# Kernel tuning notes

Hardware: AMD Instinct MI355X
Metric: run time of the kernel (lower is better)

## Reference

```python
import jax, jax.numpy as jnp
import numpy as np

N = 100000      # nodes per graph batch
E = 1600000     # edges per graph batch
F_IN = 128
HID = 128
N_GRAPHS = 64


def gcn_conv(x, edge_index, W, b):
    """PyG GCNConv: add self-loops, symmetric deg^-1/2 normalization, scatter-add."""
    n = x.shape[0]
    xw = x @ W                                  # [N, H]
    src, dst = edge_index[0], edge_index[1]
    # degree including self-loop
    deg = jnp.zeros((n,), xw.dtype).at[dst].add(jnp.ones((src.shape[0],), xw.dtype)) + 1.0
    dinv = jax.lax.rsqrt(deg)                   # deg^-1/2
    norm = (dinv[src] * dinv[dst])[:, None]     # [E, 1]
    msg = xw[src] * norm                        # gather + scale
    agg = jnp.zeros_like(xw).at[dst].add(msg)   # scatter-add
    agg = agg + xw * (dinv * dinv)[:, None]     # self-loop contribution
    return agg + b


def global_mean_pool(x, batch, num_graphs):
    sums = jax.ops.segment_sum(x, batch, num_segments=num_graphs)
    cnts = jax.ops.segment_sum(jnp.ones((x.shape[0],), x.dtype), batch, num_segments=num_graphs)
    return sums / jnp.maximum(cnts, 1.0)[:, None]


def setup_inputs() -> dict:
    key = jax.random.key(0)
    ks = jax.random.split(key, 16)
    s = 1.0 / np.sqrt(F_IN)
    sh = 1.0 / np.sqrt(HID)
    return {
        "x_H": jax.random.normal(ks[0], (N, F_IN), jnp.float32),
        "edge_index_H": jax.random.randint(ks[1], (2, E), 0, N, jnp.int64),
        "x_G": jax.random.normal(ks[2], (N, F_IN), jnp.float32),
        "edge_index_G": jax.random.randint(ks[3], (2, E), 0, N, jnp.int64),
        "batch_H": jnp.sort(jax.random.randint(ks[4], (N,), 0, N_GRAPHS, jnp.int64)),
        "batch_G": jnp.sort(jax.random.randint(ks[5], (N,), 0, N_GRAPHS, jnp.int64)),
        # selector params
        "sel_W1": jax.random.uniform(ks[6], (F_IN, HID), jnp.float32, -s, s),
        "sel_b1": jnp.zeros((HID,), jnp.float32),
        "sel_W2": jax.random.uniform(ks[7], (HID, HID), jnp.float32, -sh, sh),
        "sel_b2": jnp.zeros((HID,), jnp.float32),
        "sel_fcw": jax.random.uniform(ks[8], (HID, 1), jnp.float32, -sh, sh),
        "sel_fcb": jnp.zeros((1,), jnp.float32),
        # embedder params (shared between F and G branches)
        "emb_W1": jax.random.uniform(ks[9], (F_IN, HID), jnp.float32, -s, s),
        "emb_b1": jnp.zeros((HID,), jnp.float32),
        "emb_W2": jax.random.uniform(ks[10], (HID, HID), jnp.float32, -sh, sh),
        "emb_b2": jnp.zeros((HID,), jnp.float32),
    }


def reference(x_H, edge_index_H, x_G, edge_index_G, batch_H, batch_G,
              sel_W1, sel_b1, sel_W2, sel_b2, sel_fcw, sel_fcb,
              emb_W1, emb_b1, emb_W2, emb_b2):
    # selector on H
    h = jax.nn.relu(gcn_conv(x_H, edge_index_H, sel_W1, sel_b1))
    h = jax.nn.relu(gcn_conv(h, edge_index_H, sel_W2, sel_b2))
    p = jax.nn.sigmoid(h @ sel_fcw + sel_fcb)          # [N, 1]

    def embed(x, ei, batch):
        z = jax.nn.relu(gcn_conv(x, ei, emb_W1, emb_b1))
        z = jax.nn.relu(gcn_conv(z, ei, emb_W2, emb_b2))
        return global_mean_pool(z, batch, N_GRAPHS)

    h_F = embed(x_H * p, edge_index_H, batch_H)
    h_G = embed(x_G, edge_index_G, batch_G)
    return (h_F, h_G, p)
```

## Files before the change

### kernel.cpp

```cpp
#include <hip/hip_runtime.h>
#include <cstdint>
#include <cstddef>

#define FEAT 128
#define PSLICE 8
#define BSHIFT 7
#define CAP 4096

typedef _Float16 h16;
typedef __attribute__((ext_vector_type(8))) _Float16 h16x8;
typedef __attribute__((ext_vector_type(4))) _Float16 h16x4;
typedef __attribute__((ext_vector_type(4))) float f32x4;

__global__ __launch_bounds__(256) void k_cvt(const float* __restrict__ X,
    h16* __restrict__ Y, int nv) {
  int i = blockIdx.x * 256 + threadIdx.x;
  if (i < nv) {
    const float* p = X + (size_t)i * 8;
    float4 a = *(const float4*)p, b = *(const float4*)(p + 4);
    h16x8 o;
    o[0] = (h16)a.x; o[1] = (h16)a.y; o[2] = (h16)a.z; o[3] = (h16)a.w;
    o[4] = (h16)b.x; o[5] = (h16)b.y; o[6] = (h16)b.z; o[7] = (h16)b.w;
    *(h16x8*)&Y[(size_t)i * 8] = o;
  }
}

__global__ __launch_bounds__(256) void k_part(const int* __restrict__ ei,
    unsigned int* __restrict__ pair, int* __restrict__ gcur, int E, int nb) {
  __shared__ int cnt[1024];
  __shared__ int base[1024];
  int per = (E + gridDim.x - 1) / gridDim.x;
  int e0 = blockIdx.x * per;
  int e1 = min(e0 + per, E);
  for (int i = threadIdx.x; i < nb; i += 256) cnt[i] = 0;
  __syncthreads();
  for (int e = e0 + threadIdx.x; e < e1; e += 256)
    atomicAdd(&cnt[ei[E + e] >> BSHIFT], 1);
  __syncthreads();
  for (int i = threadIdx.x; i < nb; i += 256) {
    int c = cnt[i];
    base[i] = c ? atomicAdd(&gcur[i], c) : 0;
    cnt[i] = 0;
  }
  __syncthreads();
  for (int e = e0 + threadIdx.x; e < e1; e += 256) {
    int src = ei[e];
    int dst = ei[E + e];
    int b = dst >> BSHIFT;
    int pos = base[b] + atomicAdd(&cnt[b], 1);
    if (pos < CAP) pair[(size_t)b * CAP + pos] = ((unsigned)src << BSHIFT) | (unsigned)(dst & 127);
  }
}

__global__ __launch_bounds__(1024) void k_bscan(const int* __restrict__ cnt,
    int* __restrict__ boffs, int* __restrict__ offs, int nb, int N, int E) {
  __shared__ int wsum[16];
  __shared__ int carry;
  int tid = threadIdx.x;
  int lane = tid & 63;
  int wid = tid >> 6;
  if (tid == 0) carry = 0;
  for (int base = 0; base < nb; base += 1024) {
    __syncthreads();
    int c0 = carry;
    int i = base + tid;
    int v = (i < nb) ? cnt[i] : 0;
    int x = v;
#pragma unroll
    for (int off = 1; off < 64; off <<= 1) {
      int t = __shfl_up(x, off);
      if (lane >= off) x += t;
    }
    if (lane == 63) wsum[wid] = x;
    __syncthreads();
    if (wid == 0) {
      int t = (lane < 16) ? wsum[lane] : 0;
#pragma unroll
      for (int off = 1; off < 16; off <<= 1) {
        int u = __shfl_up(t, off);
        if (lane >= off) t += u;
      }
      if (lane < 16) wsum[lane] = t;
    }
    __syncthreads();
    int wex = (wid == 0) ? 0 : wsum[wid - 1];
    int o = c0 + wex + (x - v);
    if (i < nb) boffs[i] = o;
    int total = wsum[15];
    __syncthreads();
    if (tid == 0) carry = c0 + total;
  }
  __syncthreads();
  if (tid == 0) { boffs[nb] = carry; offs[N] = E; }
}

__global__ __launch_bounds__(256) void k_bucket(const unsigned int* __restrict__ pair,
    const int* __restrict__ bcnt, const int* __restrict__ boffs,
    int* __restrict__ csr, int* __restrict__ offs, float* __restrict__ dinv,
    int N) {
  int b = blockIdx.x;
  int m = min(bcnt[b], CAP);
  __shared__ int cnt[128];
  __shared__ int noff[128];
  __shared__ int w0tot;
  if (threadIdx.x < 128) cnt[threadIdx.x] = 0;
  __syncthreads();
  const unsigned int* p = pair + (size_t)b * CAP;
  for (int i = threadIdx.x; i < m; i += 256)
    atomicAdd(&cnt[p[i] & 127u], 1);
  __syncthreads();
  int v = 0, x = 0;
  int lane = threadIdx.x & 63, w = threadIdx.x >> 6;
  if (threadIdx.x < 128) {
    v = cnt[threadIdx.x];
    x = v;
#pragma unroll
    for (int o = 1; o < 64; o <<= 1) {
      int t = __shfl_up(x, o);
      if (lane >= o) x += t;
    }
    if (threadIdx.x == 63) w0tot = x;
  }
  __syncthreads();
  int cbase = boffs[b];
  if (threadIdx.x < 128) {
    int ex = x - v + ((w == 1) ? w0tot : 0);
    int g = (b << BSHIFT) + threadIdx.x;
    if (g < N) {
      offs[g] = cbase + ex;
      dinv[g] = 1.0f / sqrtf((float)v + 1.0f);
    }
    noff[threadIdx.x] = ex;
    cnt[threadIdx.x] = 0;
  }
  __syncthreads();
  for (int i = threadIdx.x; i < m; i += 256) {
    unsigned pk = p[i];
    int d = pk & 127u;
    int pos = cbase + noff[d] + atomicAdd(&cnt[d], 1);
    csr[pos] = (int)(pk >> BSHIFT);
  }
}

__global__ __launch_bounds__(256) void k_wprep(const float* __restrict__ W,
    h16* __restrict__ WT) {
  int i = blockIdx.x * 256 + threadIdx.x;
  int k = i >> 7, c = i & 127;
  WT[c * FEAT + k] = (h16)W[(size_t)k * FEAT + c];
}

__device__ inline float4 ldrow4(const h16* p) {
  h16x4 v = *(const h16x4*)p;
  return make_float4((float)v[0], (float)v[1], (float)v[2], (float)v[3]);
}

__device__ inline float4 gather_row(const h16* __restrict__ XW,
    const int* __restrict__ offs, const int* __restrict__ csr, int node, int f) {
  float4 a0 = ldrow4(&XW[(size_t)node * FEAT + f]);
  float4 a1 = {0,0,0,0}, a2 = {0,0,0,0}, a3 = {0,0,0,0};
  float4 a4 = {0,0,0,0}, a5 = {0,0,0,0}, a6 = {0,0,0,0}, a7 = {0,0,0,0};
  int s = offs[node], e = offs[node + 1];
  int i = s;
  for (; i + 8 <= e; i += 8) {
    int s0 = csr[i + 0], s1 = csr[i + 1], s2 = csr[i + 2], s3 = csr[i + 3];
    int s4 = csr[i + 4], s5 = csr[i + 5], s6 = csr[i + 6], s7 = csr[i + 7];
    float4 v0 = ldrow4(&XW[(size_t)s0 * FEAT + f]);
    float4 v1 = ldrow4(&XW[(size_t)s1 * FEAT + f]);
    float4 v2 = ldrow4(&XW[(size_t)s2 * FEAT + f]);
    float4 v3 = ldrow4(&XW[(size_t)s3 * FEAT + f]);
    float4 v4 = ldrow4(&XW[(size_t)s4 * FEAT + f]);
    float4 v5 = ldrow4(&XW[(size_t)s5 * FEAT + f]);
    float4 v6 = ldrow4(&XW[(size_t)s6 * FEAT + f]);
    float4 v7 = ldrow4(&XW[(size_t)s7 * FEAT + f]);
    a0.x += v0.x; a0.y += v0.y; a0.z += v0.z; a0.w += v0.w;
    a1.x += v1.x; a1.y += v1.y; a1.z += v1.z; a1.w += v1.w;
    a2.x += v2.x; a2.y += v2.y; a2.z += v2.z; a2.w += v2.w;
    a3.x += v3.x; a3.y += v3.y; a3.z += v3.z; a3.w += v3.w;
    a4.x += v4.x; a4.y += v4.y; a4.z += v4.z; a4.w += v4.w;
    a5.x += v5.x; a5.y += v5.y; a5.z += v5.z; a5.w += v5.w;
    a6.x += v6.x; a6.y += v6.y; a6.z += v6.z; a6.w += v6.w;
    a7.x += v7.x; a7.y += v7.y; a7.z += v7.z; a7.w += v7.w;
  }
  if (i + 4 <= e) {
    int s0 = csr[i + 0], s1 = csr[i + 1], s2 = csr[i + 2], s3 = csr[i + 3];
    float4 v0 = ldrow4(&XW[(size_t)s0 * FEAT + f]);
    float4 v1 = ldrow4(&XW[(size_t)s1 * FEAT + f]);
    float4 v2 = ldrow4(&XW[(size_t)s2 * FEAT + f]);
    float4 v3 = ldrow4(&XW[(size_t)s3 * FEAT + f]);
    a4.x += v0.x; a4.y += v0.y; a4.z += v0.z; a4.w += v0.w;
    a5.x += v1.x; a5.y += v1.y; a5.z += v1.z; a5.w += v1.w;
    a6.x += v2.x; a6.y += v2.y; a6.z += v2.z; a6.w += v2.w;
    a7.x += v3.x; a7.y += v3.y; a7.z += v3.z; a7.w += v3.w;
    i += 4;
  }
  for (; i < e; ++i) {
    int s0 = csr[i];
    float4 v0 = ldrow4(&XW[(size_t)s0 * FEAT + f]);
    a1.x += v0.x; a1.y += v0.y; a1.z += v0.z; a1.w += v0.w;
  }
  a0.x += a1.x; a0.y += a1.y; a0.z += a1.z; a0.w += a1.w;
  a2.x += a3.x; a2.y += a3.y; a2.z += a3.z; a2.w += a3.w;
  a4.x += a5.x; a4.y += a5.y; a4.z += a5.z; a4.w += a5.w;
  a6.x += a7.x; a6.y += a7.y; a6.z += a7.z; a6.w += a7.w;
  a0.x += a2.x; a0.y += a2.y; a0.z += a2.z; a0.w += a2.w;
  a4.x += a6.x; a4.y += a6.y; a4.z += a6.z; a4.w += a6.w;
  a0.x += a4.x; a0.y += a4.y; a0.z += a4.z; a0.w += a4.w;
  return a0;
}

__global__ __launch_bounds__(256) void k_agg(const h16* __restrict__ XW,
    const int* __restrict__ offs, const int* __restrict__ csr,
    const float* __restrict__ dinv, const float* __restrict__ bias,
    h16* __restrict__ out, int n) {
  int half = threadIdx.x >> 5;
  int lane = threadIdx.x & 31;
  int node = blockIdx.x * 8 + half;
  if (node >= n) return;
  int f = lane * 4;
  float4 a = gather_row(XW, offs, csr, node, f);
  float d = dinv[node];
  float4 b = *(const float4*)&bias[f];
  h16x4 o;
  o[0] = (h16)fmaxf(a.x * d + b.x, 0.f);
  o[1] = (h16)fmaxf(a.y * d + b.y, 0.f);
  o[2] = (h16)fmaxf(a.z * d + b.z, 0.f);
  o[3] = (h16)fmaxf(a.w * d + b.w, 0.f);
  *(h16x4*)&out[(size_t)node * FEAT + f] = o;
}

__global__ __launch_bounds__(256) void k_agg_pvec(const h16* __restrict__ XW,
    const int* __restrict__ offs, const int* __restrict__ csr,
    const float* __restrict__ dinv, const float* __restrict__ bias,
    const float* __restrict__ fcw, const float* __restrict__ fcb,
    float* __restrict__ p, int n) {
  int half = threadIdx.x >> 5;
  int lane = threadIdx.x & 31;
  int node = blockIdx.x * 8 + half;
  if (node >= n) return;
  int f = lane * 4;
  float4 a = gather_row(XW, offs, csr, node, f);
  float d = dinv[node];
  float4 b = *(const float4*)&bias[f];
  float4 wv = *(const float4*)&fcw[f];
  float acc = fmaxf(a.x * d + b.x, 0.f) * wv.x
            + fmaxf(a.y * d + b.y, 0.f) * wv.y
            + fmaxf(a.z * d + b.z, 0.f) * wv.z
            + fmaxf(a.w * d + b.w, 0.f) * wv.w;
#pragma unroll
  for (int off = 16; off > 0; off >>= 1) acc += __shfl_xor(acc, off, 32);
  if (lane == 0) p[node] = 1.0f / (1.0f + expf(-(acc + fcb[0])));
}

__device__ inline h16x8 load8(const float* p) {
  float4 a = *(const float4*)p, b = *(const float4*)(p + 4);
  h16x8 o;
  o[0] = (h16)a.x; o[1] = (h16)a.y; o[2] = (h16)a.z; o[3] = (h16)a.w;
  o[4] = (h16)b.x; o[5] = (h16)b.y; o[6] = (h16)b.z; o[7] = (h16)b.w;
  return o;
}
__device__ inline h16x8 load8(const h16* p) { return *(const h16x8*)p; }

template <typename TI>
__global__ __launch_bounds__(256) void k_gemm_mfma(const TI* __restrict__ X,
    const h16* __restrict__ WT, const float* __restrict__ s1, const float* __restrict__ s2,
    h16* __restrict__ Y, int n) {
  __shared__ __align__(16) h16 lA[128 * FEAT];
  __shared__ __align__(16) h16 lB[128 * FEAT];
  int tid = threadIdx.x;
  int row0 = blockIdx.x * 128;
#pragma unroll
  for (int i = 0; i < 8; ++i) {
    int c = tid + i * 256;
    int r = c >> 4, kc = c & 15;
    int grow = row0 + r;
    h16x8 v;
#pragma unroll
    for (int j = 0; j < 8; ++j) v[j] = (h16)0.f;
    if (grow < n) v = load8(&X[(size_t)grow * FEAT + kc * 8]);
    int byte = r * 256 + ((kc * 16) ^ ((r & 7) << 4));
    *(h16x8*)((char*)lA + byte) = v;
  }
#pragma unroll
  for (int i = 0; i < 8; ++i) {
    int c = tid + i * 256;
    int col = c >> 4, kc = c & 15;
    h16x8 v = *(const h16x8*)&WT[col * FEAT + kc * 8];
    int byte = col * 256 + ((kc * 16) ^ ((col & 7) << 4));
    *(h16x8*)((char*)lB + byte) = v;
  }
  __syncthreads();
  int w = tid >> 6, l = tid & 63;
  int lr = l & 15, lq = l >> 4;
  h16x8 af[2][4];
#pragma unroll
  for (int m = 0; m < 2; ++m)
#pragma unroll
    for (int s = 0; s < 4; ++s) {
      int r = w * 32 + m * 16 + lr;
      int k2 = (s * 32 + lq * 8) * 2;
      int byte = r * 256 + (k2 ^ ((r & 7) << 4));
      af[m][s] = *(const h16x8*)((const char*)lA + byte);
    }
  f32x4 acc[2][8];
#pragma unroll
  for (int m = 0; m < 2; ++m)
#pragma unroll
    for (int nn = 0; nn < 8; ++nn) acc[m][nn] = (f32x4){0.f, 0.f, 0.f, 0.f};
#pragma unroll
  for (int nn = 0; nn < 8; ++nn) {
#pragma unroll
    for (int s = 0; s < 4; ++s) {
      int col = nn * 16 + lr;
      int k2 = (s * 32 + lq * 8) * 2;
      int byte = col * 256 + (k2 ^ ((col & 7) << 4));
      h16x8 bf = *(const h16x8*)((const char*)lB + byte);
      acc[0][nn] = __builtin_amdgcn_mfma_f32_16x16x32_f16(af[0][s], bf, acc[0][nn], 0, 0, 0);
      acc[1][nn] = __builtin_amdgcn_mfma_f32_16x16x32_f16(af[1][s], bf, acc[1][nn], 0, 0, 0);
    }
  }
#pragma unroll
  for (int m = 0; m < 2; ++m) {
#pragma unroll
    for (int r = 0; r < 4; ++r) {
      int grow = row0 + w * 32 + m * 16 + lq * 4 + r;
      if (grow < n) {
        float sc = 1.0f;
        if (s1) sc = s1[grow];
        if (s2) sc *= s2[grow];
#pragma unroll
        for (int nn = 0; nn < 8; ++nn)
          Y[(size_t)grow * FEAT + nn * 16 + lr] = (h16)(acc[m][nn][r] * sc);
      }
    }
  }
}

__global__ __launch_bounds__(256) void k_pool_part(const h16* __restrict__ Z,
    const int* __restrict__ batch, float* __restrict__ part, int n) {
  int g = blockIdx.x / PSLICE;
  int s = blockIdx.x % PSLICE;
  int lo = 0, hi = n;
  while (lo < hi) { int m = (lo + hi) >> 1; if (batch[m] < g) lo = m + 1; else hi = m; }
  int start = lo;
  hi = n;
  while (lo < hi) { int m = (lo + hi) >> 1; if (batch[m] <= g) lo = m + 1; else hi = m; }
  int end = lo;
  int len = end - start;
  int per = (len + PSLICE - 1) / PSLICE;
  int r0 = start + s * per;
  int r1 = min(r0 + per, end);
  int f = threadIdx.x & 127;
  int half = threadIdx.x >> 7;
  float acc = 0.f;
  for (int i = r0 + half; i < r1; i += 2) acc += (float)Z[(size_t)i * FEAT + f];
  __shared__ float lds[256];
  lds[threadIdx.x] = acc;
  __syncthreads();
  if (half == 0) part[(size_t)blockIdx.x * FEAT + f] = lds[f] + lds[128 + f];
}

__global__ __launch_bounds__(128) void k_pool_fin(const float* __restrict__ part,
    const int* __restrict__ batch, float* __restrict__ out, int n) {
  int g = blockIdx.x;
  int lo = 0, hi = n;
  while (lo < hi) { int m = (lo + hi) >> 1; if (batch[m] < g) lo = m + 1; else hi = m; }
  int start = lo;
  hi = n;
  while (lo < hi) { int m = (lo + hi) >> 1; if (batch[m] <= g) lo = m + 1; else hi = m; }
  int len = lo - start;
  int f = threadIdx.x;
  float tot = 0.f;
#pragma unroll
  for (int s = 0; s < PSLICE; ++s) tot += part[(size_t)(g * PSLICE + s) * FEAT + f];
  out[(size_t)g * FEAT + f] = tot / fmaxf((float)len, 1.0f);
}

extern "C" void kernel_launch(void* const* d_in, const int* in_sizes, int n_in,
                              void* d_out, int out_size, void* d_ws, size_t ws_size,
                              hipStream_t stream) {
  const float* x_H    = (const float*)d_in[0];
  const int*   ei_H   = (const int*)d_in[1];
  const float* x_G    = (const float*)d_in[2];
  const int*   ei_G   = (const int*)d_in[3];
  const int*   bat_H  = (const int*)d_in[4];
  const int*   bat_G  = (const int*)d_in[5];
  const float* sel_W1 = (const float*)d_in[6];
  const float* sel_b1 = (const float*)d_in[7];
  const float* sel_W2 = (const float*)d_in[8];
  const float* sel_b2 = (const float*)d_in[9];
  const float* sel_fcw = (const float*)d_in[10];
  const float* sel_fcb = (const float*)d_in[11];
  const float* emb_W1 = (const float*)d_in[12];
  const float* emb_b1 = (const float*)d_in[13];
  const float* emb_W2 = (const float*)d_in[14];
  const float* emb_b2 = (const float*)d_in[15];

  const int N = in_sizes[0] / FEAT;
  const int E = in_sizes[1] / 2;
  const int NG = 64;
  const int NB = (N + 127) >> BSHIFT;

  float* out = (float*)d_out;
  float* hF = out;
  float* hG = out + NG * FEAT;
  float* p  = out + 2 * NG * FEAT;

  char* ws = (char*)d_ws;
  size_t off = 0;
  auto alloc = [&](size_t bytes) -> void* {
    void* ptr = (void*)(ws + off);
    off += (bytes + 511) & ~(size_t)511;
    return ptr;
  };
  const size_t SZH = (size_t)N * FEAT * sizeof(h16);
  const size_t SZP = (size_t)NB * CAP * sizeof(unsigned int);
  const size_t SZB = SZH > SZP ? SZH : SZP;
  h16* A       = (h16*)alloc(SZB);
  h16* B       = (h16*)alloc(SZB);
  h16* C       = (h16*)alloc(SZH);
  h16* x16H    = (h16*)alloc(SZH);
  float* dinvH = (float*)alloc((size_t)N * 4);
  float* dinvG = (float*)alloc((size_t)N * 4);
  int*  offsH  = (int*)alloc((size_t)(N + 1) * 4);
  int*  offsG  = (int*)alloc((size_t)(N + 1) * 4);
  int*  csrH   = (int*)alloc((size_t)E * 4);
  int*  csrG   = (int*)alloc((size_t)E * 4);
  int*  gcurH  = (int*)alloc((size_t)NB * 4);
  int*  gcurG  = (int*)alloc((size_t)NB * 4);
  int*  boffsH = (int*)alloc((size_t)(NB + 1) * 4);
  int*  boffsG = (int*)alloc((size_t)(NB + 1) * 4);
  float* part  = (float*)alloc((size_t)NG * PSLICE * FEAT * 4);
  h16* wtSel1  = (h16*)alloc((size_t)FEAT * FEAT * 2);
  h16* wtSel2  = (h16*)alloc((size_t)FEAT * FEAT * 2);
  h16* wtEmb1  = (h16*)alloc((size_t)FEAT * FEAT * 2);
  h16* wtEmb2  = (h16*)alloc((size_t)FEAT * FEAT * 2);
  (void)ws_size;

  unsigned int* pairH = (unsigned int*)A;
  unsigned int* pairG = (unsigned int*)B;

  const int gGemm = (N + 127) / 128;
  const int gAgg  = (N + 7) / 8;

  k_wprep<<<64, 256, 0, stream>>>(sel_W1, wtSel1);
  k_wprep<<<64, 256, 0, stream>>>(sel_W2, wtSel2);
  k_wprep<<<64, 256, 0, stream>>>(emb_W1, wtEmb1);
  k_wprep<<<64, 256, 0, stream>>>(emb_W2, wtEmb2);
  k_cvt<<<(N * FEAT / 8 + 255) / 256, 256, 0, stream>>>(x_H, x16H, N * FEAT / 8);

  hipMemsetAsync(gcurH, 0, (size_t)NB * 4, stream);
  hipMemsetAsync(gcurG, 0, (size_t)NB * 4, stream);
  k_part<<<256, 256, 0, stream>>>(ei_H, pairH, gcurH, E, NB);
  k_part<<<256, 256, 0, stream>>>(ei_G, pairG, gcurG, E, NB);
  k_bscan<<<1, 1024, 0, stream>>>(gcurH, boffsH, offsH, NB, N, E);
  k_bscan<<<1, 1024, 0, stream>>>(gcurG, boffsG, offsG, NB, N, E);
  k_bucket<<<NB, 256, 0, stream>>>(pairH, gcurH, boffsH, csrH, offsH, dinvH, N);
  k_bucket<<<NB, 256, 0, stream>>>(pairG, gcurG, boffsG, csrG, offsG, dinvG, N);

  k_gemm_mfma<h16><<<gGemm, 256, 0, stream>>>(x16H, wtSel1, dinvH, nullptr, A, N);
  k_agg<<<gAgg, 256, 0, stream>>>(A, offsH, csrH, dinvH, sel_b1, B, N);
  k_gemm_mfma<h16><<<gGemm, 256, 0, stream>>>(B, wtSel2, dinvH, nullptr, C, N);
  k_agg_pvec<<<gAgg, 256, 0, stream>>>(C, offsH, csrH, dinvH, sel_b2, sel_fcw, sel_fcb, p, N);

  k_gemm_mfma<h16><<<gGemm, 256, 0, stream>>>(x16H, wtEmb1, dinvH, p, A, N);
  k_agg<<<gAgg, 256, 0, stream>>>(A, offsH, csrH, dinvH, emb_b1, B, N);
  k_gemm_mfma<h16><<<gGemm, 256, 0, stream>>>(B, wtEmb2, dinvH, nullptr, C, N);
  k_agg<<<gAgg, 256, 0, stream>>>(C, offsH, csrH, dinvH, emb_b2, B, N);
  k_pool_part<<<NG * PSLICE, 256, 0, stream>>>(B, bat_H, part, N);
  k_pool_fin<<<NG, 128, 0, stream>>>(part, bat_H, hF, N);

  k_gemm_mfma<float><<<gGemm, 256, 0, stream>>>(x_G, wtEmb1, dinvG, nullptr, A, N);
  k_agg<<<gAgg, 256, 0, stream>>>(A, offsG, csrG, dinvG, emb_b1, B, N);
  k_gemm_mfma<h16><<<gGemm, 256, 0, stream>>>(B, wtEmb2, dinvG, nullptr, C, N);
  k_agg<<<gAgg, 256, 0, stream>>>(C, offsG, csrG, dinvG, emb_b2, B, N);
  k_pool_part<<<NG * PSLICE, 256, 0, stream>>>(B, bat_G, part, N);
  k_pool_fin<<<NG, 128, 0, stream>>>(part, bat_G, hG, N);
}
```

Before: 709.5 us.

## Widen aggregation gathers to 16B per lane and fuse final aggregation into mean pooling

```diff
diff --git a/kernel.cpp b/kernel.cpp
--- a/kernel.cpp
+++ b/kernel.cpp
@@ -3,13 +3,12 @@
 #include <cstddef>
 
 #define FEAT 128
-#define PSLICE 8
+#define PSL2 32
 #define BSHIFT 7
 #define CAP 4096
 
 typedef _Float16 h16;
 typedef __attribute__((ext_vector_type(8))) _Float16 h16x8;
-typedef __attribute__((ext_vector_type(4))) _Float16 h16x4;
 typedef __attribute__((ext_vector_type(4))) float f32x4;
 
 __global__ __launch_bounds__(256) void k_cvt(const float* __restrict__ X,
@@ -149,83 +148,86 @@
   WT[c * FEAT + k] = (h16)W[(size_t)k * FEAT + c];
 }
 
-__device__ inline float4 ldrow4(const h16* p) {
-  h16x4 v = *(const h16x4*)p;
-  return make_float4((float)v[0], (float)v[1], (float)v[2], (float)v[3]);
-}
-
-__device__ inline float4 gather_row(const h16* __restrict__ XW,
-    const int* __restrict__ offs, const int* __restrict__ csr, int node, int f) {
-  float4 a0 = ldrow4(&XW[(size_t)node * FEAT + f]);
-  float4 a1 = {0,0,0,0}, a2 = {0,0,0,0}, a3 = {0,0,0,0};
-  float4 a4 = {0,0,0,0}, a5 = {0,0,0,0}, a6 = {0,0,0,0}, a7 = {0,0,0,0};
+__device__ inline void acc8(f32x4& lo, f32x4& hi, h16x8 v) {
+  lo[0] += (float)v[0]; lo[1] += (float)v[1]; lo[2] += (float)v[2]; lo[3] += (float)v[3];
+  hi[0] += (float)v[4]; hi[1] += (float)v[5]; hi[2] += (float)v[6]; hi[3] += (float)v[7];
+}
+
+__device__ inline void gather_row8(const h16* __restrict__ XW,
+    const int* __restrict__ offs, const int* __restrict__ csr,
+    int node, int f0, f32x4& olo, f32x4& ohi) {
+  f32x4 lo0 = {0,0,0,0}, hi0 = {0,0,0,0};
+  f32x4 lo1 = {0,0,0,0}, hi1 = {0,0,0,0};
+  f32x4 lo2 = {0,0,0,0}, hi2 = {0,0,0,0};
+  f32x4 lo3 = {0,0,0,0}, hi3 = {0,0,0,0};
+  h16x8 sv = *(const h16x8*)&XW[(size_t)node * FEAT + f0];
+  acc8(lo0, hi0, sv);
   int s = offs[node], e = offs[node + 1];
   int i = s;
   for (; i + 8 <= e; i += 8) {
     int s0 = csr[i + 0], s1 = csr[i + 1], s2 = csr[i + 2], s3 = csr[i + 3];
     int s4 = csr[i + 4], s5 = csr[i + 5], s6 = csr[i + 6], s7 = csr[i + 7];
-    float4 v0 = ldrow4(&XW[(size_t)s0 * FEAT + f]);
-    float4 v1 = ldrow4(&XW[(size_t)s1 * FEAT + f]);
-    float4 v2 = ldrow4(&XW[(size_t)s2 * FEAT + f]);
-    float4 v3 = ldrow4(&XW[(size_t)s3 * FEAT + f]);
-    float4 v4 = ldrow4(&XW[(size_t)s4 * FEAT + f]);
-    float4 v5 = ldrow4(&XW[(size_t)s5 * FEAT + f]);
-    float4 v6 = ldrow4(&XW[(size_t)s6 * FEAT + f]);
-    float4 v7 = ldrow4(&XW[(size_t)s7 * FEAT + f]);
-    a0.x += v0.x; a0.y += v0.y; a0.z += v0.z; a0.w += v0.w;
-    a1.x += v1.x; a1.y += v1.y; a1.z += v1.z; a1.w += v1.w;
-    a2.x += v2.x; a2.y += v2.y; a2.z += v2.z; a2.w += v2.w;
-    a3.x += v3.x; a3.y += v3.y; a3.z += v3.z; a3.w += v3.w;
-    a4.x += v4.x; a4.y += v4.y; a4.z += v4.z; a4.w += v4.w;
-    a5.x += v5.x; a5.y += v5.y; a5.z += v5.z; a5.w += v5.w;
-    a6.x += v6.x; a6.y += v6.y; a6.z += v6.z; a6.w += v6.w;
-    a7.x += v7.x; a7.y += v7.y; a7.z += v7.z; a7.w += v7.w;
+    h16x8 v0 = *(const h16x8*)&XW[(size_t)s0 * FEAT + f0];
+    h16x8 v1 = *(const h16x8*)&XW[(size_t)s1 * FEAT + f0];
+    h16x8 v2 = *(const h16x8*)&XW[(size_t)s2 * FEAT + f0];
+    h16x8 v3 = *(const h16x8*)&XW[(size_t)s3 * FEAT + f0];
+    h16x8 v4 = *(const h16x8*)&XW[(size_t)s4 * FEAT + f0];
+    h16x8 v5 = *(const h16x8*)&XW[(size_t)s5 * FEAT + f0];
+    h16x8 v6 = *(const h16x8*)&XW[(size_t)s6 * FEAT + f0];
+    h16x8 v7 = *(const h16x8*)&XW[(size_t)s7 * FEAT + f0];
+    acc8(lo0, hi0, v0); acc8(lo1, hi1, v1);
+    acc8(lo2, hi2, v2); acc8(lo3, hi3, v3);
+    acc8(lo0, hi0, v4); acc8(lo1, hi1, v5);
+    acc8(lo2, hi2, v6); acc8(lo3, hi3, v7);
   }
   if (i + 4 <= e) {
     int s0 = csr[i + 0], s1 = csr[i + 1], s2 = csr[i + 2], s3 = csr[i + 3];
-    float4 v0 = ldrow4(&XW[(size_t)s0 * FEAT + f]);
-    float4 v1 = ldrow4(&XW[(size_t)s1 * FEAT + f]);
-    float4 v2 = ldrow4(&XW[(size_t)s2 * FEAT + f]);
-    float4 v3 = ldrow4(&XW[(size_t)s3 * FEAT + f]);
-    a4.x += v0.x; a4.y += v0.y; a4.z += v0.z; a4.w += v0.w;
-    a5.x += v1.x; a5.y += v1.y; a5.z += v1.z; a5.w += v1.w;
-    a6.x += v2.x; a6.y += v2.y; a6.z += v2.z; a6.w += v2.w;
-    a7.x += v3.x; a7.y += v3.y; a7.z += v3.z; a7.w += v3.w;
+    h16x8 v0 = *(const h16x8*)&XW[(size_t)s0 * FEAT + f0];
+    h16x8 v1 = *(const h16x8*)&XW[(size_t)s1 * FEAT + f0];
+    h16x8 v2 = *(const h16x8*)&XW[(size_t)s2 * FEAT + f0];
+    h16x8 v3 = *(const h16x8*)&XW[(size_t)s3 * FEAT + f0];
+    acc8(lo0, hi0, v0); acc8(lo1, hi1, v1);
+    acc8(lo2, hi2, v2); acc8(lo3, hi3, v3);
     i += 4;
   }
   for (; i < e; ++i) {
     int s0 = csr[i];
-    float4 v0 = ldrow4(&XW[(size_t)s0 * FEAT + f]);
-    a1.x += v0.x; a1.y += v0.y; a1.z += v0.z; a1.w += v0.w;
-  }
-  a0.x += a1.x; a0.y += a1.y; a0.z += a1.z; a0.w += a1.w;
-  a2.x += a3.x; a2.y += a3.y; a2.z += a3.z; a2.w += a3.w;
-  a4.x += a5.x; a4.y += a5.y; a4.z += a5.z; a4.w += a5.w;
-  a6.x += a7.x; a6.y += a7.y; a6.z += a7.z; a6.w += a7.w;
-  a0.x += a2.x; a0.y += a2.y; a0.z += a2.z; a0.w += a2.w;
-  a4.x += a6.x; a4.y += a6.y; a4.z += a6.z; a4.w += a6.w;
-  a0.x += a4.x; a0.y += a4.y; a0.z += a4.z; a0.w += a4.w;
-  return a0;
+    h16x8 v0 = *(const h16x8*)&XW[(size_t)s0 * FEAT + f0];
+    acc8(lo1, hi1, v0);
+  }
+  lo0[0]+=lo1[0]; lo0[1]+=lo1[1]; lo0[2]+=lo1[2]; lo0[3]+=lo1[3];
+  hi0[0]+=hi1[0]; hi0[1]+=hi1[1]; hi0[2]+=hi1[2]; hi0[3]+=hi1[3];
+  lo2[0]+=lo3[0]; lo2[1]+=lo3[1]; lo2[2]+=lo3[2]; lo2[3]+=lo3[3];
+  hi2[0]+=hi3[0]; hi2[1]+=hi3[1]; hi2[2]+=hi3[2]; hi2[3]+=hi3[3];
+  lo0[0]+=lo2[0]; lo0[1]+=lo2[1]; lo0[2]+=lo2[2]; lo0[3]+=lo2[3];
+  hi0[0]+=hi2[0]; hi0[1]+=hi2[1]; hi0[2]+=hi2[2]; hi0[3]+=hi2[3];
+  olo = lo0; ohi = hi0;
 }
 
 __global__ __launch_bounds__(256) void k_agg(const h16* __restrict__ XW,
     const int* __restrict__ offs, const int* __restrict__ csr,
     const float* __restrict__ dinv, const float* __restrict__ bias,
     h16* __restrict__ out, int n) {
-  int half = threadIdx.x >> 5;
-  int lane = threadIdx.x & 31;
-  int node = blockIdx.x * 8 + half;
+  int gid = threadIdx.x >> 4;
+  int lane = threadIdx.x & 15;
+  int node = blockIdx.x * 16 + gid;
   if (node >= n) return;
-  int f = lane * 4;
-  float4 a = gather_row(XW, offs, csr, node, f);
+  int f0 = lane * 8;
+  f32x4 lo, hi;
+  gather_row8(XW, offs, csr, node, f0, lo, hi);
   float d = dinv[node];
-  float4 b = *(const float4*)&bias[f];
-  h16x4 o;
-  o[0] = (h16)fmaxf(a.x * d + b.x, 0.f);
-  o[1] = (h16)fmaxf(a.y * d + b.y, 0.f);
-  o[2] = (h16)fmaxf(a.z * d + b.z, 0.f);
-  o[3] = (h16)fmaxf(a.w * d + b.w, 0.f);
-  *(h16x4*)&out[(size_t)node * FEAT + f] = o;
+  float4 b0 = *(const float4*)&bias[f0];
+  float4 b1 = *(const float4*)&bias[f0 + 4];
+  h16x8 o;
+  o[0] = (h16)fmaxf(lo[0] * d + b0.x, 0.f);
+  o[1] = (h16)fmaxf(lo[1] * d + b0.y, 0.f);
+  o[2] = (h16)fmaxf(lo[2] * d + b0.z, 0.f);
+  o[3] = (h16)fmaxf(lo[3] * d + b0.w, 0.f);
+  o[4] = (h16)fmaxf(hi[0] * d + b1.x, 0.f);
+  o[5] = (h16)fmaxf(hi[1] * d + b1.y, 0.f);
+  o[6] = (h16)fmaxf(hi[2] * d + b1.z, 0.f);
+  o[7] = (h16)fmaxf(hi[3] * d + b1.w, 0.f);
+  *(h16x8*)&out[(size_t)node * FEAT + f0] = o;
 }
 
 __global__ __launch_bounds__(256) void k_agg_pvec(const h16* __restrict__ XW,
@@ -233,130 +235,77 @@
     const float* __restrict__ dinv, const float* __restrict__ bias,
     const float* __restrict__ fcw, const float* __restrict__ fcb,
     float* __restrict__ p, int n) {
-  int half = threadIdx.x >> 5;
-  int lane = threadIdx.x & 31;
-  int node = blockIdx.x * 8 + half;
+  int gid = threadIdx.x >> 4;
+  int lane = threadIdx.x & 15;
+  int node = blockIdx.x * 16 + gid;
   if (node >= n) return;
-  int f = lane * 4;
-  float4 a = gather_row(XW, offs, csr, node, f);
+  int f0 = lane * 8;
+  f32x4 lo, hi;
+  gather_row8(XW, offs, csr, node, f0, lo, hi);
   float d = dinv[node];
-  float4 b = *(const float4*)&bias[f];
-  float4 wv = *(const float4*)&fcw[f];
-  float acc = fmaxf(a.x * d + b.x, 0.f) * wv.x
-            + fmaxf(a.y * d + b.y, 0.f) * wv.y
-            + fmaxf(a.z * d + b.z, 0.f) * wv.z
-            + fmaxf(a.w * d + b.w, 0.f) * wv.w;
-#pragma unroll
-  for (int off = 16; off > 0; off >>= 1) acc += __shfl_xor(acc, off, 32);
+  float4 b0 = *(const float4*)&bias[f0];
+  float4 b1 = *(const float4*)&bias[f0 + 4];
+  float4 w0 = *(const float4*)&fcw[f0];
+  float4 w1 = *(const float4*)&fcw[f0 + 4];
+  float acc = fmaxf(lo[0] * d + b0.x, 0.f) * w0.x
+            + fmaxf(lo[1] * d + b0.y, 0.f) * w0.y
+            + fmaxf(lo[2] * d + b0.z, 0.f) * w0.z
+            + fmaxf(lo[3] * d + b0.w, 0.f) * w0.w
+            + fmaxf(hi[0] * d + b1.x, 0.f) * w1.x
+            + fmaxf(hi[1] * d + b1.y, 0.f) * w1.y
+            + fmaxf(hi[2] * d + b1.z, 0.f) * w1.z
+            + fmaxf(hi[3] * d + b1.w, 0.f) * w1.w;
+#pragma unroll
+  for (int off = 8; off > 0; off >>= 1) acc += __shfl_xor(acc, off, 16);
   if (lane == 0) p[node] = 1.0f / (1.0f + expf(-(acc + fcb[0])));
 }
 
-__device__ inline h16x8 load8(const float* p) {
-  float4 a = *(const float4*)p, b = *(const float4*)(p + 4);
-  h16x8 o;
-  o[0] = (h16)a.x; o[1] = (h16)a.y; o[2] = (h16)a.z; o[3] = (h16)a.w;
-  o[4] = (h16)b.x; o[5] = (h16)b.y; o[6] = (h16)b.z; o[7] = (h16)b.w;
-  return o;
-}
-__device__ inline h16x8 load8(const h16* p) { return *(const h16x8*)p; }
-
-template <typename TI>
-__global__ __launch_bounds__(256) void k_gemm_mfma(const TI* __restrict__ X,
-    const h16* __restrict__ WT, const float* __restrict__ s1, const float* __restrict__ s2,
-    h16* __restrict__ Y, int n) {
-  __shared__ __align__(16) h16 lA[128 * FEAT];
-  __shared__ __align__(16) h16 lB[128 * FEAT];
-  int tid = threadIdx.x;
-  int row0 = blockIdx.x * 128;
-#pragma unroll
-  for (int i = 0; i < 8; ++i) {
-    int c = tid + i * 256;
-    int r = c >> 4, kc = c & 15;
-    int grow = row0 + r;
-    h16x8 v;
-#pragma unroll
-    for (int j = 0; j < 8; ++j) v[j] = (h16)0.f;
-    if (grow < n) v = load8(&X[(size_t)grow * FEAT + kc * 8]);
-    int byte = r * 256 + ((kc * 16) ^ ((r & 7) << 4));
-    *(h16x8*)((char*)lA + byte) = v;
-  }
-#pragma unroll
-  for (int i = 0; i < 8; ++i) {
-    int c = tid + i * 256;
-    int col = c >> 4, kc = c & 15;
-    h16x8 v = *(const h16x8*)&WT[col * FEAT + kc * 8];
-    int byte = col * 256 + ((kc * 16) ^ ((col & 7) << 4));
-    *(h16x8*)((char*)lB + byte) = v;
-  }
-  __syncthreads();
-  int w = tid >> 6, l = tid & 63;
-  int lr = l & 15, lq = l >> 4;
-  h16x8 af[2][4];
-#pragma unroll
-  for (int m = 0; m < 2; ++m)
-#pragma unroll
-    for (int s = 0; s < 4; ++s) {
-      int r = w * 32 + m * 16 + lr;
-      int k2 = (s * 32 + lq * 8) * 2;
-      int byte = r * 256 + (k2 ^ ((r & 7) << 4));
-      af[m][s] = *(const h16x8*)((const char*)lA + byte);
-    }
-  f32x4 acc[2][8];
-#pragma unroll
-  for (int m = 0; m < 2; ++m)
-#pragma unroll
-    for (int nn = 0; nn < 8; ++nn) acc[m][nn] = (f32x4){0.f, 0.f, 0.f, 0.f};
-#pragma unroll
-  for (int nn = 0; nn < 8; ++nn) {
-#pragma unroll
-    for (int s = 0; s < 4; ++s) {
-      int col = nn * 16 + lr;
-      int k2 = (s * 32 + lq * 8) * 2;
-      int byte = col * 256 + (k2 ^ ((col & 7) << 4));
-      h16x8 bf = *(const h16x8*)((const char*)lB + byte);
-      acc[0][nn] = __builtin_amdgcn_mfma_f32_16x16x32_f16(af[0][s], bf, acc[0][nn], 0, 0, 0);
-      acc[1][nn] = __builtin_amdgcn_mfma_f32_16x16x32_f16(af[1][s], bf, acc[1][nn], 0, 0, 0);
-    }
-  }
-#pragma unroll
-  for (int m = 0; m < 2; ++m) {
-#pragma unroll
-    for (int r = 0; r < 4; ++r) {
-      int grow = row0 + w * 32 + m * 16 + lq * 4 + r;
-      if (grow < n) {
-        float sc = 1.0f;
-        if (s1) sc = s1[grow];
-        if (s2) sc *= s2[grow];
-#pragma unroll
-        for (int nn = 0; nn < 8; ++nn)
-          Y[(size_t)grow * FEAT + nn * 16 + lr] = (h16)(acc[m][nn][r] * sc);
-      }
-    }
-  }
-}
-
-__global__ __launch_bounds__(256) void k_pool_part(const h16* __restrict__ Z,
+__global__ __launch_bounds__(256) void k_agg_pool(const h16* __restrict__ XW,
+    const int* __restrict__ offs, const int* __restrict__ csr,
+    const float* __restrict__ dinv, const float* __restrict__ bias,
     const int* __restrict__ batch, float* __restrict__ part, int n) {
-  int g = blockIdx.x / PSLICE;
-  int s = blockIdx.x % PSLICE;
-  int lo = 0, hi = n;
-  while (lo < hi) { int m = (lo + hi) >> 1; if (batch[m] < g) lo = m + 1; else hi = m; }
-  int start = lo;
-  hi = n;
-  while (lo < hi) { int m = (lo + hi) >> 1; if (batch[m] <= g) lo = m + 1; else hi = m; }
-  int end = lo;
+  int g = blockIdx.x / PSL2;
+  int s = blockIdx.x % PSL2;
+  int lo_ = 0, hi_ = n;
+  while (lo_ < hi_) { int m = (lo_ + hi_) >> 1; if (batch[m] < g) lo_ = m + 1; else hi_ = m; }
+  int start = lo_;
+  hi_ = n;
+  while (lo_ < hi_) { int m = (lo_ + hi_) >> 1; if (batch[m] <= g) lo_ = m + 1; else hi_ = m; }
+  int end = lo_;
   int len = end - start;
-  int per = (len + PSLICE - 1) / PSLICE;
+  int per = (len + PSL2 - 1) / PSL2;
   int r0 = start + s * per;
   int r1 = min(r0 + per, end);
-  int f = threadIdx.x & 127;
-  int half = threadIdx.x >> 7;
-  float acc = 0.f;
-  for (int i = r0 + half; i < r1; i += 2) acc += (float)Z[(size_t)i * FEAT + f];
-  __shared__ float lds[256];
-  lds[threadIdx.x] = acc;
-  __syncthreads();
-  if (half == 0) part[(size_t)blockIdx.x * FEAT + f] = lds[f] + lds[128 + f];
+  int gid = threadIdx.x >> 4;
+  int lane = threadIdx.x & 15;
+  int f0 = lane * 8;
+  float4 b0 = *(const float4*)&bias[f0];
+  float4 b1 = *(const float4*)&bias[f0 + 4];
+  f32x4 plo = {0,0,0,0}, phi = {0,0,0,0};
+  for (int node = r0 + gid; node < r1; node += 16) {
+    f32x4 lo, hi;
+    gather_row8(XW, offs, csr, node, f0, lo, hi);
+    float d = dinv[node];
+    plo[0] += fmaxf(lo[0] * d + b0.x, 0.f);
+    plo[1] += fmaxf(lo[1] * d + b0.y, 0.f);
+    plo[2] += fmaxf(lo[2] * d + b0.z, 0.f);
+    plo[3] += fmaxf(lo[3] * d + b0.w, 0.f);
+    phi[0] += fmaxf(hi[0] * d + b1.x, 0.f);
+    phi[1] += fmaxf(hi[1] * d + b1.y, 0.f);
+    phi[2] += fmaxf(hi[2] * d + b1.z, 0.f);
+    phi[3] += fmaxf(hi[3] * d + b1.w, 0.f);
+  }
+  __shared__ float lds[16 * FEAT];
+  *(f32x4*)&lds[gid * FEAT + f0] = plo;
+  *(f32x4*)&lds[gid * FEAT + f0 + 4] = phi;
+  __syncthreads();
+  if (threadIdx.x < FEAT) {
+    int f = threadIdx.x;
+    float t = 0.f;
+#pragma unroll
+    for (int q = 0; q < 16; ++q) t += lds[q * FEAT + f];
+    part[(size_t)blockIdx.x * FEAT + f] = t;
+  }
 }
 
 __global__ __launch_bounds__(128) void k_pool_fin(const float* __restrict__ part,
@@ -371,8 +320,92 @@
   int f = threadIdx.x;
   float tot = 0.f;
 #pragma unroll
-  for (int s = 0; s < PSLICE; ++s) tot += part[(size_t)(g * PSLICE + s) * FEAT + f];
+  for (int s = 0; s < PSL2; ++s) tot += part[(size_t)(g * PSL2 + s) * FEAT + f];
   out[(size_t)g * FEAT + f] = tot / fmaxf((float)len, 1.0f);
+}
+
+__device__ inline h16x8 load8(const float* p) {
+  float4 a = *(const float4*)p, b = *(const float4*)(p + 4);
+  h16x8 o;
+  o[0] = (h16)a.x; o[1] = (h16)a.y; o[2] = (h16)a.z; o[3] = (h16)a.w;
+  o[4] = (h16)b.x; o[5] = (h16)b.y; o[6] = (h16)b.z; o[7] = (h16)b.w;
+  return o;
+}
+__device__ inline h16x8 load8(const h16* p) { return *(const h16x8*)p; }
+
+template <typename TI>
+__global__ __launch_bounds__(256) void k_gemm_mfma(const TI* __restrict__ X,
+    const h16* __restrict__ WT, const float* __restrict__ s1, const float* __restrict__ s2,
+    h16* __restrict__ Y, int n) {
+  __shared__ __align__(16) h16 lA[128 * FEAT];
+  __shared__ __align__(16) h16 lB[128 * FEAT];
+  int tid = threadIdx.x;
+  int row0 = blockIdx.x * 128;
+#pragma unroll
+  for (int i = 0; i < 8; ++i) {
+    int c = tid + i * 256;
+    int r = c >> 4, kc = c & 15;
+    int grow = row0 + r;
+    h16x8 v;
+#pragma unroll
+    for (int j = 0; j < 8; ++j) v[j] = (h16)0.f;
+    if (grow < n) v = load8(&X[(size_t)grow * FEAT + kc * 8]);
+    int byte = r * 256 + ((kc * 16) ^ ((r & 7) << 4));
+    *(h16x8*)((char*)lA + byte) = v;
+  }
+#pragma unroll
+  for (int i = 0; i < 8; ++i) {
+    int c = tid + i * 256;
+    int col = c >> 4, kc = c & 15;
+    h16x8 v = *(const h16x8*)&WT[col * FEAT + kc * 8];
+    int byte = col * 256 + ((kc * 16) ^ ((col & 7) << 4));
+    *(h16x8*)((char*)lB + byte) = v;
+  }
+  __syncthreads();
+  int w = tid >> 6, l = tid & 63;
+  int lr = l & 15, lq = l >> 4;
+  h16x8 af[2][4];
+#pragma unroll
+  for (int m = 0; m < 2; ++m)
+#pragma unroll
+    for (int s = 0; s < 4; ++s) {
+      int r = w * 32 + m * 16 + lr;
+      int k2 = (s * 32 + lq * 8) * 2;
+      int byte = r * 256 + (k2 ^ ((r & 7) << 4));
+      af[m][s] = *(const h16x8*)((const char*)lA + byte);
+    }
+  f32x4 acc[2][8];
+#pragma unroll
+  for (int m = 0; m < 2; ++m)
+#pragma unroll
+    for (int nn = 0; nn < 8; ++nn) acc[m][nn] = (f32x4){0.f, 0.f, 0.f, 0.f};
+#pragma unroll
+  for (int nn = 0; nn < 8; ++nn) {
+#pragma unroll
+    for (int s = 0; s < 4; ++s) {
+      int col = nn * 16 + lr;
+      int k2 = (s * 32 + lq * 8) * 2;
+      int byte = col * 256 + (k2 ^ ((col & 7) << 4));
+      h16x8 bf = *(const h16x8*)((const char*)lB + byte);
+      acc[0][nn] = __builtin_amdgcn_mfma_f32_16x16x32_f16(af[0][s], bf, acc[0][nn], 0, 0, 0);
+      acc[1][nn] = __builtin_amdgcn_mfma_f32_16x16x32_f16(af[1][s], bf, acc[1][nn], 0, 0, 0);
+    }
+  }
+#pragma unroll
+  for (int m = 0; m < 2; ++m) {
+#pragma unroll
+    for (int r = 0; r < 4; ++r) {
+      int grow = row0 + w * 32 + m * 16 + lq * 4 + r;
+      if (grow < n) {
+        float sc = 1.0f;
+        if (s1) sc = s1[grow];
+        if (s2) sc *= s2[grow];
+#pragma unroll
+        for (int nn = 0; nn < 8; ++nn)
+          Y[(size_t)grow * FEAT + nn * 16 + lr] = (h16)(acc[m][nn][r] * sc);
+      }
+    }
+  }
 }
 
 extern "C" void kernel_launch(void* const* d_in, const int* in_sizes, int n_in,
@@ -429,7 +462,7 @@
   int*  gcurG  = (int*)alloc((size_t)NB * 4);
   int*  boffsH = (int*)alloc((size_t)(NB + 1) * 4);
   int*  boffsG = (int*)alloc((size_t)(NB + 1) * 4);
-  float* part  = (float*)alloc((size_t)NG * PSLICE * FEAT * 4);
+  float* part  = (float*)alloc((size_t)NG * PSL2 * FEAT * 4);
   h16* wtSel1  = (h16*)alloc((size_t)FEAT * FEAT * 2);
   h16* wtSel2  = (h16*)alloc((size_t)FEAT * FEAT * 2);
   h16* wtEmb1  = (h16*)alloc((size_t)FEAT * FEAT * 2);
@@ -440,7 +473,7 @@
   unsigned int* pairG = (unsigned int*)B;
 
   const int gGemm = (N + 127) / 128;
-  const int gAgg  = (N + 7) / 8;
+  const int gAgg  = (N + 15) / 16;
 
   k_wprep<<<64, 256, 0, stream>>>(sel_W1, wtSel1);
   k_wprep<<<64, 256, 0, stream>>>(sel_W2, wtSel2);
@@ -465,14 +498,12 @@
   k_gemm_mfma<h16><<<gGemm, 256, 0, stream>>>(x16H, wtEmb1, dinvH, p, A, N);
   k_agg<<<gAgg, 256, 0, stream>>>(A, offsH, csrH, dinvH, emb_b1, B, N);
   k_gemm_mfma<h16><<<gGemm, 256, 0, stream>>>(B, wtEmb2, dinvH, nullptr, C, N);
-  k_agg<<<gAgg, 256, 0, stream>>>(C, offsH, csrH, dinvH, emb_b2, B, N);
-  k_pool_part<<<NG * PSLICE, 256, 0, stream>>>(B, bat_H, part, N);
+  k_agg_pool<<<NG * PSL2, 256, 0, stream>>>(C, offsH, csrH, dinvH, emb_b2, bat_H, part, N);
   k_pool_fin<<<NG, 128, 0, stream>>>(part, bat_H, hF, N);
 
   k_gemm_mfma<float><<<gGemm, 256, 0, stream>>>(x_G, wtEmb1, dinvG, nullptr, A, N);
   k_agg<<<gAgg, 256, 0, stream>>>(A, offsG, csrG, dinvG, emb_b1, B, N);
   k_gemm_mfma<h16><<<gGemm, 256, 0, stream>>>(B, wtEmb2, dinvG, nullptr, C, N);
-  k_agg<<<gAgg, 256, 0, stream>>>(C, offsG, csrG, dinvG, emb_b2, B, N);
-  k_pool_part<<<NG * PSLICE, 256, 0, stream>>>(B, bat_G, part, N);
+  k_agg_pool<<<NG * PSL2, 256, 0, stream>>>(C, offsG, csrG, dinvG, emb_b2, bat_G, part, N);
   k_pool_fin<<<NG, 128, 0, stream>>>(part, bat_G, hG, N);
 }
```

New measurement: 639.3 us (median of 2 runs). 9.9% less time.
